# Performance work log

Measured on AMD Instinct MI355X. Metric: run time of the kernel, lower is better.

The kernel has to match this reference:

```python
import jax, jax.numpy as jnp
import numpy as np

N_NODES = 100000
N_EDGES = 1600000
D = 64
N_TARGETS = 100
N_GRAPHS = 512


def gcn_conv(x, W, b, src, dst):
    """GCNConv with default add_self_loops=True, symmetric normalization."""
    n = x.shape[0]
    h = x @ W  # [N, out]
    ones = jnp.ones(dst.shape[0], dtype=h.dtype)
    deg = jax.ops.segment_sum(ones, dst, num_segments=n) + 1.0  # +1 for self-loop
    dinv = jax.lax.rsqrt(deg)
    norm = dinv[src] * dinv[dst]  # [E]
    agg = jax.ops.segment_sum(h[src] * norm[:, None], dst, num_segments=n)
    agg = agg + h * (dinv * dinv)[:, None]  # self-loop contribution: 1/deg[i] * h[i]
    return agg + b


def setup_inputs() -> dict:
    key = jax.random.key(0)
    ks = jax.random.split(key, 12)
    x = jax.random.normal(ks[0], (N_NODES, D), dtype=jnp.float32)
    edge_index = jax.random.randint(ks[1], (2, N_EDGES), 0, N_NODES, dtype=jnp.int64)
    batch_seg = jnp.sort(jax.random.randint(ks[2], (N_NODES,), 0, N_GRAPHS, dtype=jnp.int64))
    s = 1.0 / np.sqrt(D)
    W1 = jax.random.normal(ks[3], (D, D), dtype=jnp.float32) * s
    b1 = jnp.zeros((D,), dtype=jnp.float32)
    W2 = jax.random.normal(ks[4], (D, D), dtype=jnp.float32) * s
    b2 = jnp.zeros((D,), dtype=jnp.float32)
    W3 = jax.random.normal(ks[5], (D, D), dtype=jnp.float32) * s
    b3 = jnp.zeros((D,), dtype=jnp.float32)
    Wout = jax.random.normal(ks[6], (D, N_TARGETS), dtype=jnp.float32) * s
    bout = jnp.zeros((N_TARGETS,), dtype=jnp.float32)
    return {"x": x, "W1": W1, "b1": b1, "W2": W2, "b2": b2, "W3": W3, "b3": b3,
            "Wout": Wout, "bout": bout, "edge_index": edge_index, "batch_seg": batch_seg}


def reference(x, W1, b1, W2, b2, W3, b3, Wout, bout, edge_index, batch_seg):
    src, dst = edge_index[0], edge_index[1]
    h = jax.nn.relu(gcn_conv(x, W1, b1, src, dst))   # dropout p=0 -> identity
    h = jax.nn.relu(gcn_conv(h, W2, b2, src, dst))
    h = gcn_conv(h, W3, b3, src, dst)
    counts = jax.ops.segment_sum(jnp.ones(h.shape[0], h.dtype), batch_seg, num_segments=N_GRAPHS)
    pooled = jax.ops.segment_sum(h, batch_seg, num_segments=N_GRAPHS) / jnp.maximum(counts, 1.0)[:, None]
    return pooled @ Wout + bout  # [N_GRAPHS, N_TARGETS]
```

## Files before the change

kernel.cpp:

```cpp
#include <hip/hip_runtime.h>

#define N_NODES   100000
#define N_EDGES   1600000
#define D         64
#define N_TARGETS 100
#define N_GRAPHS  512
#define NBUCK     391
#define EPB       4096
#define BCAP      6144
#define MM_NPW    16
#define NPN       4

typedef _Float16 half4 __attribute__((ext_vector_type(4)));
typedef _Float16 half8 __attribute__((ext_vector_type(8)));
typedef __fp16   hf2   __attribute__((ext_vector_type(2)));
typedef __fp16   hf8   __attribute__((ext_vector_type(8)));

#if defined(__has_builtin)
#if __has_builtin(__builtin_amdgcn_fdot2)
#define USE_DOT2 1
#endif
#endif

__global__ void k_init(int* __restrict__ gcur, float* __restrict__ poolz) {
    int i = blockIdx.x * blockDim.x + threadIdx.x;
    if (i < NBUCK) gcur[i] = 0;
    if (i < N_GRAPHS * D + N_GRAPHS) poolz[i] = 0.0f;
}

__global__ void k_prepW(const float* __restrict__ W, _Float16* __restrict__ out) {
    int t = threadIdx.x;
#pragma unroll
    for (int it = 0; it < 2; ++it) {
        int idx = t + it * 256;
        int m = idx >> 3, c = idx & 7;
        half8 hv;
#pragma unroll
        for (int tt = 0; tt < 8; ++tt)
            hv[tt] = (_Float16)W[(8 * c + tt) * 64 + m];
        *(half8*)&out[m * 64 + ((c ^ (m & 7)) * 8)] = hv;
    }
}

__global__ void __launch_bounds__(256)
k_binA(const int* __restrict__ src, const int* __restrict__ dst,
       int* __restrict__ gcur, unsigned long long* __restrict__ staged) {
    __shared__ int hist[NBUCK];
    __shared__ int boff[NBUCK];
    int tid = threadIdx.x;
    for (int i = tid; i < NBUCK; i += 256) hist[i] = 0;
    __syncthreads();

    int e0 = blockIdx.x * EPB;
    int s_[16], d_[16], r_[16];
#pragma unroll
    for (int k = 0; k < 16; ++k) {
        int e = e0 + k * 256 + tid;
        if (e < N_EDGES) {
            s_[k] = src[e];
            d_[k] = dst[e];
            r_[k] = atomicAdd(&hist[d_[k] >> 8], 1);
        } else {
            d_[k] = -1;
        }
    }
    __syncthreads();
    for (int b = tid; b < NBUCK; b += 256) {
        int h = hist[b];
        boff[b] = (h > 0) ? atomicAdd(&gcur[b], h) : 0;
    }
    __syncthreads();
#pragma unroll
    for (int k = 0; k < 16; ++k) {
        if (d_[k] >= 0) {
            int b = d_[k] >> 8;
            staged[(size_t)b * BCAP + boff[b] + r_[k]] =
                ((unsigned long long)(unsigned)d_[k] << 32) | (unsigned)s_[k];
        }
    }
}

__global__ void k_scanB(const int* __restrict__ gcur, int* __restrict__ bstart) {
    __shared__ int s[512];
    int t = threadIdx.x;
    int v = (t < NBUCK) ? gcur[t] : 0;
    s[t] = v;
    __syncthreads();
    for (int off = 1; off < 512; off <<= 1) {
        int x = (t >= off) ? s[t - off] : 0;
        __syncthreads();
        s[t] += x;
        __syncthreads();
    }
    if (t < NBUCK) bstart[t] = s[t] - v;
    if (t == 0) bstart[NBUCK] = N_EDGES;
}

__global__ void __launch_bounds__(256)
k_binB(const unsigned long long* __restrict__ staged, const int* __restrict__ gcur,
       const int* __restrict__ bstart, int* __restrict__ esrc,
       int* __restrict__ base, float* __restrict__ dinv) {
    __shared__ int s[256];
    __shared__ int lbase[256];
    __shared__ int cur[256];
    int b = blockIdx.x;
    int t = threadIdx.x;
    int n0 = b << 8;
    int Eb = gcur[b];
    int Sb = bstart[b];
    const unsigned long long* sl = staged + (size_t)b * BCAP;

    cur[t] = 0;
    __syncthreads();
    for (int k = t; k < Eb; k += 256) {
        int dl = ((int)(sl[k] >> 32)) & 255;
        atomicAdd(&cur[dl], 1);
    }
    __syncthreads();
    int v = cur[t];
    s[t] = v;
    __syncthreads();
    for (int off = 1; off < 256; off <<= 1) {
        int x = (t >= off) ? s[t - off] : 0;
        __syncthreads();
        s[t] += x;
        __syncthreads();
    }
    lbase[t] = s[t] - v;
    int gi = n0 + t;
    if (gi < N_NODES) {
        base[gi] = Sb + (s[t] - v);
        dinv[gi] = rsqrtf((float)v + 1.0f);
    }
    if (b == 0 && t == 0) base[N_NODES] = N_EDGES;
    cur[t] = 0;
    __syncthreads();
    for (int k = t; k < Eb; k += 256) {
        unsigned long long pd = sl[k];
        int dl = ((int)(pd >> 32)) & 255;
        int pos = Sb + lbase[dl] + atomicAdd(&cur[dl], 1);
        esrc[pos] = (int)(pd & 0xffffffffu);
    }
}

__global__ void __launch_bounds__(256)
k_mm(const float* __restrict__ X, const float* __restrict__ W,
     const float* __restrict__ dinv, _Float16* __restrict__ Y16) {
    __shared__ float W1L[D * D];
    __shared__ float aSh[4][D];
    int tid = threadIdx.x;
#pragma unroll
    for (int it = 0; it < 4; ++it) {
        int idx = (tid + it * 256) * 4;
        *(float4*)&W1L[idx] = *(const float4*)(W + idx);
    }
    __syncthreads();

    int wv = tid >> 6, lane = tid & 63;
    float wreg[D];
#pragma unroll
    for (int k = 0; k < D; ++k)
        wreg[k] = W1L[k * D + lane];

    int i0 = (blockIdx.x * 4 + wv) * MM_NPW;
    if (i0 >= N_NODES) return;
    int iEnd = i0 + MM_NPW; if (iEnd > N_NODES) iEnd = N_NODES;

    float xv = X[(size_t)i0 * D + lane];
    for (int i = i0; i < iEnd; ++i) {
        int inext = (i + 1 < N_NODES) ? (i + 1) : i;
        float xnext = X[(size_t)inext * D + lane];

        aSh[wv][lane] = xv;
        asm volatile("s_waitcnt lgkmcnt(0)" ::: "memory");

        float ac0 = 0.f, ac1 = 0.f, ac2 = 0.f, ac3 = 0.f;
#pragma unroll
        for (int c = 0; c < 16; ++c) {
            float4 a4 = *(const float4*)&aSh[wv][c * 4];
            ac0 = fmaf(a4.x, wreg[4 * c + 0], ac0);
            ac1 = fmaf(a4.y, wreg[4 * c + 1], ac1);
            ac2 = fmaf(a4.z, wreg[4 * c + 2], ac2);
            ac3 = fmaf(a4.w, wreg[4 * c + 3], ac3);
        }
        float acc = (ac0 + ac1) + (ac2 + ac3);
        Y16[(size_t)i * D + lane] = (_Float16)(acc * dinv[i]);
        xv = xnext;
    }
}

__global__ void __launch_bounds__(256)
k_pullmm(const _Float16* __restrict__ H, const int* __restrict__ esrc,
         const int* __restrict__ base, const float* __restrict__ dinv,
         const float* __restrict__ b_in, const _Float16* __restrict__ Whg,
         _Float16* __restrict__ Hout) {
    __shared__ _Float16 WhL[D * D];
    __shared__ float    red[4][8][D + 4];
    __shared__ _Float16 aSh[4][D];
    {
#pragma unroll
        for (int it = 0; it < 2; ++it) {
            int t = threadIdx.x + it * 256;
            *(half8*)&WhL[t * 8] = *(const half8*)&Whg[t * 8];
        }
    }
    __syncthreads();

    int wv   = threadIdx.x >> 6;
    int lane = threadIdx.x & 63;
    int g = lane >> 3, l = lane & 7;
    float bias = b_in[lane];
    int i0 = (blockIdx.x * 4 + wv) * NPN;

    for (int n = 0; n < NPN; ++n) {
        int i = i0 + n;
        int s0 = base[i], s1 = base[i + 1];

        float acc[8] = {0.f, 0.f, 0.f, 0.f, 0.f, 0.f, 0.f, 0.f};
        if (g == 0) {
            half8 sv = *(const half8*)(H + (size_t)i * D + l * 8);
#pragma unroll
            for (int q = 0; q < 8; ++q) acc[q] = (float)sv[q];
        }

        int p = s0;
        while (p < s1) {
            int cnt = s1 - p;
            if (cnt > 64) cnt = 64;
            int ed = (lane < cnt) ? esrc[p + lane] : 0;
            int j = 0;
            for (; j + 32 <= cnt; j += 32) {
                int e0 = __shfl(ed, j + g, 64);
                int e1 = __shfl(ed, j + 8 + g, 64);
                int e2 = __shfl(ed, j + 16 + g, 64);
                int e3 = __shfl(ed, j + 24 + g, 64);
                half8 v0 = *(const half8*)(H + (size_t)(unsigned)e0 * D + l * 8);
                half8 v1 = *(const half8*)(H + (size_t)(unsigned)e1 * D + l * 8);
                half8 v2 = *(const half8*)(H + (size_t)(unsigned)e2 * D + l * 8);
                half8 v3 = *(const half8*)(H + (size_t)(unsigned)e3 * D + l * 8);
                half8 s01 = v0 + v1;
                half8 s23 = v2 + v3;
#pragma unroll
                for (int q = 0; q < 8; ++q)
                    acc[q] += (float)s01[q] + (float)s23[q];
            }
            for (; j + 16 <= cnt; j += 16) {
                int e0 = __shfl(ed, j + g, 64);
                int e1 = __shfl(ed, j + 8 + g, 64);
                half8 v0 = *(const half8*)(H + (size_t)(unsigned)e0 * D + l * 8);
                half8 v1 = *(const half8*)(H + (size_t)(unsigned)e1 * D + l * 8);
                half8 s01 = v0 + v1;
#pragma unroll
                for (int q = 0; q < 8; ++q) acc[q] += (float)s01[q];
            }
            for (; j + 8 <= cnt; j += 8) {
                int e0 = __shfl(ed, j + g, 64);
                half8 v0 = *(const half8*)(H + (size_t)(unsigned)e0 * D + l * 8);
#pragma unroll
                for (int q = 0; q < 8; ++q) acc[q] += (float)v0[q];
            }
            if (j < cnt) {
                int idx = j + g;
                int e0 = __shfl(ed, idx & 63, 64);
                if (idx < cnt) {
                    half8 v0 = *(const half8*)(H + (size_t)(unsigned)e0 * D + l * 8);
#pragma unroll
                    for (int q = 0; q < 8; ++q) acc[q] += (float)v0[q];
                }
            }
            p += cnt;
        }

        *(float4*)&red[wv][g][l * 8]     = make_float4(acc[0], acc[1], acc[2], acc[3]);
        *(float4*)&red[wv][g][l * 8 + 4] = make_float4(acc[4], acc[5], acc[6], acc[7]);
        asm volatile("s_waitcnt lgkmcnt(0)" ::: "memory");
        float agg = 0.f;
#pragma unroll
        for (int gg = 0; gg < 8; ++gg)
            agg += red[wv][gg][lane];

        float di = dinv[i];
        float av = fmaxf(fmaf(agg, di, bias), 0.f);
        aSh[wv][lane] = (_Float16)av;
        asm volatile("s_waitcnt lgkmcnt(0)" ::: "memory");

        float part = 0.f;
#pragma unroll
        for (int c = 0; c < 8; ++c) {
            hf8 a8 = *(const hf8*)&aSh[wv][c * 8];
            hf8 w8 = *(const hf8*)&WhL[lane * 64 + ((c ^ (lane & 7)) * 8)];
#ifdef USE_DOT2
#pragma unroll
            for (int q = 0; q < 4; ++q) {
                hf2 ap; ap.x = a8[2 * q]; ap.y = a8[2 * q + 1];
                hf2 wp; wp.x = w8[2 * q]; wp.y = w8[2 * q + 1];
                part = __builtin_amdgcn_fdot2(ap, wp, part, false);
            }
#else
#pragma unroll
            for (int t = 0; t < 8; ++t)
                part = fmaf((float)a8[t], (float)w8[t], part);
#endif
        }
        Hout[(size_t)i * D + lane] = (_Float16)(part * di);
    }
}

__global__ void __launch_bounds__(256)
k_pull(const _Float16* __restrict__ H, const int* __restrict__ esrc,
       const int* __restrict__ base, const float* __restrict__ dinv,
       const float* __restrict__ b, _Float16* __restrict__ AGG16) {
    __shared__ float red[4][8][D + 4];
    int wv   = threadIdx.x >> 6;
    int lane = threadIdx.x & 63;
    int g = lane >> 3, l = lane & 7;
    float bias = b[lane];
    int i0 = (blockIdx.x * 4 + wv) * NPN;

    for (int n = 0; n < NPN; ++n) {
        int i = i0 + n;
        int s0 = base[i], s1 = base[i + 1];

        float acc[8] = {0.f, 0.f, 0.f, 0.f, 0.f, 0.f, 0.f, 0.f};
        if (g == 0) {
            half8 sv = *(const half8*)(H + (size_t)i * D + l * 8);
#pragma unroll
            for (int q = 0; q < 8; ++q) acc[q] = (float)sv[q];
        }

        int p = s0;
        while (p < s1) {
            int cnt = s1 - p;
            if (cnt > 64) cnt = 64;
            int ed = (lane < cnt) ? esrc[p + lane] : 0;
            int j = 0;
            for (; j + 32 <= cnt; j += 32) {
                int e0 = __shfl(ed, j + g, 64);
                int e1 = __shfl(ed, j + 8 + g, 64);
                int e2 = __shfl(ed, j + 16 + g, 64);
                int e3 = __shfl(ed, j + 24 + g, 64);
                half8 v0 = *(const half8*)(H + (size_t)(unsigned)e0 * D + l * 8);
                half8 v1 = *(const half8*)(H + (size_t)(unsigned)e1 * D + l * 8);
                half8 v2 = *(const half8*)(H + (size_t)(unsigned)e2 * D + l * 8);
                half8 v3 = *(const half8*)(H + (size_t)(unsigned)e3 * D + l * 8);
                half8 s01 = v0 + v1;
                half8 s23 = v2 + v3;
#pragma unroll
                for (int q = 0; q < 8; ++q)
                    acc[q] += (float)s01[q] + (float)s23[q];
            }
            for (; j + 16 <= cnt; j += 16) {
                int e0 = __shfl(ed, j + g, 64);
                int e1 = __shfl(ed, j + 8 + g, 64);
                half8 v0 = *(const half8*)(H + (size_t)(unsigned)e0 * D + l * 8);
                half8 v1 = *(const half8*)(H + (size_t)(unsigned)e1 * D + l * 8);
                half8 s01 = v0 + v1;
#pragma unroll
                for (int q = 0; q < 8; ++q) acc[q] += (float)s01[q];
            }
            for (; j + 8 <= cnt; j += 8) {
                int e0 = __shfl(ed, j + g, 64);
                half8 v0 = *(const half8*)(H + (size_t)(unsigned)e0 * D + l * 8);
#pragma unroll
                for (int q = 0; q < 8; ++q) acc[q] += (float)v0[q];
            }
            if (j < cnt) {
                int idx = j + g;
                int e0 = __shfl(ed, idx & 63, 64);
                if (idx < cnt) {
                    half8 v0 = *(const half8*)(H + (size_t)(unsigned)e0 * D + l * 8);
#pragma unroll
                    for (int q = 0; q < 8; ++q) acc[q] += (float)v0[q];
                }
            }
            p += cnt;
        }

        *(float4*)&red[wv][g][l * 8]     = make_float4(acc[0], acc[1], acc[2], acc[3]);
        *(float4*)&red[wv][g][l * 8 + 4] = make_float4(acc[4], acc[5], acc[6], acc[7]);
        asm volatile("s_waitcnt lgkmcnt(0)" ::: "memory");
        float agg = 0.f;
#pragma unroll
        for (int gg = 0; gg < 8; ++gg)
            agg += red[wv][gg][lane];
        asm volatile("s_waitcnt lgkmcnt(0)" ::: "memory");

        AGG16[(size_t)i * D + lane] = (_Float16)fmaf(agg, dinv[i], bias);
    }
}

__global__ void __launch_bounds__(256)
k_pool_seg(const _Float16* __restrict__ H16, const int* __restrict__ seg,
           float* __restrict__ pooled, float* __restrict__ counts) {
    int wave = threadIdx.x >> 6;
    int lane = threadIdx.x & 63;
    int n0 = (blockIdx.x * 4 + wave) * 64;
    if (n0 >= N_NODES) return;
    int nEnd = n0 + 64;
    if (nEnd > N_NODES) nEnd = N_NODES;
    int cur = seg[n0];
    float acc = 0.0f;
    int run = 0;
    for (int n = n0; n < nEnd; ++n) {
        int gsg = seg[n];
        if (gsg != cur) {
            atomicAdd(&pooled[(size_t)cur * D + lane], acc);
            if (lane == 0) atomicAdd(&counts[cur], (float)run);
            acc = 0.0f; run = 0;
            cur = gsg;
        }
        acc += (float)H16[(size_t)n * D + lane];
        run += 1;
    }
    atomicAdd(&pooled[(size_t)cur * D + lane], acc);
    if (lane == 0) atomicAdd(&counts[cur], (float)run);
}

__global__ void k_out(const float* __restrict__ pooled, const float* __restrict__ counts,
                      const float* __restrict__ Wout, const float* __restrict__ bout,
                      float* __restrict__ out) {
    __shared__ float prow[D];
    int g = blockIdx.x;
    int t = threadIdx.x;
    if (t < D) prow[t] = pooled[(size_t)g * D + t] / fmaxf(counts[g], 1.0f);
    __syncthreads();
    if (t < N_TARGETS) {
        float acc = bout[t];
#pragma unroll
        for (int k = 0; k < D; ++k)
            acc = fmaf(prow[k], Wout[k * N_TARGETS + t], acc);
        out[g * N_TARGETS + t] = acc;
    }
}


extern "C" void kernel_launch(void* const* d_in, const int* in_sizes, int n_in,
                              void* d_out, int out_size, void* d_ws, size_t ws_size,
                              hipStream_t stream) {
    const float* x    = (const float*)d_in[0];
    const float* W1   = (const float*)d_in[1];
    const float* b1   = (const float*)d_in[2];
    const float* W2   = (const float*)d_in[3];
    const float* b2   = (const float*)d_in[4];
    const float* W3   = (const float*)d_in[5];
    const float* b3   = (const float*)d_in[6];
    const float* Wout = (const float*)d_in[7];
    const float* bout = (const float*)d_in[8];
    const int*   eidx = (const int*)d_in[9];
    const int*   seg  = (const int*)d_in[10];
    const int* src = eidx;
    const int* dst = eidx + N_EDGES;
    float* out = (float*)d_out;

    _Float16* H16A   = (_Float16*)d_ws;
    _Float16* H16B   = H16A + (size_t)N_NODES * D;
    _Float16* AGG16  = H16B;
    unsigned long long* staged = (unsigned long long*)d_ws;
    int*      esrc   = (int*)(H16B + (size_t)N_NODES * D);
    float*    dinv   = (float*)(esrc + N_EDGES);
    int*      base   = (int*)(dinv + N_NODES);
    float*    pooled = (float*)(base + N_NODES + 4);
    float*    counts = pooled + N_GRAPHS * D;
    int*      gcur   = (int*)(counts + N_GRAPHS);
    int*      bstart = gcur + 512;
    _Float16* WhA    = (_Float16*)(bstart + 512);
    _Float16* WhB    = WhA + 4096;

    const int NB = (N_NODES + 255) / 256;

    k_prepW<<<1, 256, 0, stream>>>(W2, WhA);
    k_prepW<<<1, 256, 0, stream>>>(W3, WhB);

    k_init<<<130, 256, 0, stream>>>(gcur, pooled);
    k_binA<<<(N_EDGES + EPB - 1) / EPB, 256, 0, stream>>>(src, dst, gcur, staged);
    k_scanB<<<1, 512, 0, stream>>>(gcur, bstart);
    k_binB<<<NBUCK, 256, 0, stream>>>(staged, gcur, bstart, esrc, base, dinv);

    const int MMB = (N_NODES + 4 * MM_NPW - 1) / (4 * MM_NPW);
    const int PB  = N_NODES / (4 * NPN);
    k_mm<<<MMB, 256, 0, stream>>>(x, W1, dinv, H16A);
    k_pullmm<<<PB, 256, 0, stream>>>(H16A, esrc, base, dinv, b1, WhA, H16B);
    k_pullmm<<<PB, 256, 0, stream>>>(H16B, esrc, base, dinv, b2, WhB, H16A);
    k_pull<<<PB, 256, 0, stream>>>(H16A, esrc, base, dinv, b3, AGG16);

    k_pool_seg<<<NB, 256, 0, stream>>>(AGG16, seg, pooled, counts);
    k_out<<<N_GRAPHS, 128, 0, stream>>>(pooled, counts, Wout, bout, out);
}
```

Measured before the change: 320.2 us.

## Fuse mean-pool into final pull kernel and prefetch next node's edges

The last aggregation kernel now accumulates each node's output directly into per-graph pooled sums with atomics, so the fp16 intermediate buffer and the separate pooling kernel go away. Both pull kernels also preload all node base offsets and prefetch the next node's edge-index chunk and self row while the current node is processed, to hide gather latency. In exchange, the number of pooling atomics grows, since each wave flushes after only four nodes, which adds contention on the pooled rows.

```diff
diff --git a/kernel.cpp b/kernel.cpp
--- a/kernel.cpp
+++ b/kernel.cpp
@@ -212,22 +212,37 @@
     float bias = b_in[lane];
     int i0 = (blockIdx.x * 4 + wv) * NPN;
 
+    int bv[NPN + 1];
+#pragma unroll
+    for (int q = 0; q <= NPN; ++q) bv[q] = base[i0 + q];
+
+    int pc0 = bv[1] - bv[0]; if (pc0 > 64) pc0 = 64;
+    int edn = (lane < pc0) ? esrc[bv[0] + lane] : 0;
+    half8 svn = *(const half8*)(H + (size_t)i0 * D + l * 8);
+
+#pragma unroll
     for (int n = 0; n < NPN; ++n) {
         int i = i0 + n;
-        int s0 = base[i], s1 = base[i + 1];
+        int s0 = bv[n], s1 = bv[n + 1];
+        int ed0 = edn;
+        half8 sv = svn;
+
+        if (n + 1 < NPN) {
+            int pcN = bv[n + 2] - bv[n + 1]; if (pcN > 64) pcN = 64;
+            edn = (lane < pcN) ? esrc[bv[n + 1] + lane] : 0;
+            svn = *(const half8*)(H + (size_t)(i + 1) * D + l * 8);
+        }
 
         float acc[8] = {0.f, 0.f, 0.f, 0.f, 0.f, 0.f, 0.f, 0.f};
         if (g == 0) {
-            half8 sv = *(const half8*)(H + (size_t)i * D + l * 8);
 #pragma unroll
             for (int q = 0; q < 8; ++q) acc[q] = (float)sv[q];
         }
 
         int p = s0;
+        int cnt = s1 - p; if (cnt > 64) cnt = 64;
+        int ed = ed0;
         while (p < s1) {
-            int cnt = s1 - p;
-            if (cnt > 64) cnt = 64;
-            int ed = (lane < cnt) ? esrc[p + lane] : 0;
             int j = 0;
             for (; j + 32 <= cnt; j += 32) {
                 int e0 = __shfl(ed, j + g, 64);
@@ -269,6 +284,9 @@
                 }
             }
             p += cnt;
+            if (p >= s1) break;
+            cnt = s1 - p; if (cnt > 64) cnt = 64;
+            ed = (lane < cnt) ? esrc[p + lane] : 0;
         }
 
         *(float4*)&red[wv][g][l * 8]     = make_float4(acc[0], acc[1], acc[2], acc[3]);
@@ -309,7 +327,8 @@
 __global__ void __launch_bounds__(256)
 k_pull(const _Float16* __restrict__ H, const int* __restrict__ esrc,
        const int* __restrict__ base, const float* __restrict__ dinv,
-       const float* __restrict__ b, _Float16* __restrict__ AGG16) {
+       const float* __restrict__ b, const int* __restrict__ seg,
+       float* __restrict__ pooled, float* __restrict__ counts) {
     __shared__ float red[4][8][D + 4];
     int wv   = threadIdx.x >> 6;
     int lane = threadIdx.x & 63;
@@ -317,22 +336,44 @@
     float bias = b[lane];
     int i0 = (blockIdx.x * 4 + wv) * NPN;
 
+    int bv[NPN + 1];
+#pragma unroll
+    for (int q = 0; q <= NPN; ++q) bv[q] = base[i0 + q];
+    int sgv[NPN];
+#pragma unroll
+    for (int q = 0; q < NPN; ++q) sgv[q] = seg[i0 + q];
+
+    int pc0 = bv[1] - bv[0]; if (pc0 > 64) pc0 = 64;
+    int edn = (lane < pc0) ? esrc[bv[0] + lane] : 0;
+    half8 svn = *(const half8*)(H + (size_t)i0 * D + l * 8);
+
+    int   curs = sgv[0];
+    float poolacc = 0.f;
+    int   run = 0;
+
+#pragma unroll
     for (int n = 0; n < NPN; ++n) {
         int i = i0 + n;
-        int s0 = base[i], s1 = base[i + 1];
+        int s0 = bv[n], s1 = bv[n + 1];
+        int ed0 = edn;
+        half8 sv = svn;
+
+        if (n + 1 < NPN) {
+            int pcN = bv[n + 2] - bv[n + 1]; if (pcN > 64) pcN = 64;
+            edn = (lane < pcN) ? esrc[bv[n + 1] + lane] : 0;
+            svn = *(const half8*)(H + (size_t)(i + 1) * D + l * 8);
+        }
 
         float acc[8] = {0.f, 0.f, 0.f, 0.f, 0.f, 0.f, 0.f, 0.f};
         if (g == 0) {
-            half8 sv = *(const half8*)(H + (size_t)i * D + l * 8);
 #pragma unroll
             for (int q = 0; q < 8; ++q) acc[q] = (float)sv[q];
         }
 
         int p = s0;
+        int cnt = s1 - p; if (cnt > 64) cnt = 64;
+        int ed = ed0;
         while (p < s1) {
-            int cnt = s1 - p;
-            if (cnt > 64) cnt = 64;
-            int ed = (lane < cnt) ? esrc[p + lane] : 0;
             int j = 0;
             for (; j + 32 <= cnt; j += 32) {
                 int e0 = __shfl(ed, j + g, 64);
@@ -374,6 +415,9 @@
                 }
             }
             p += cnt;
+            if (p >= s1) break;
+            cnt = s1 - p; if (cnt > 64) cnt = 64;
+            ed = (lane < cnt) ? esrc[p + lane] : 0;
         }
 
         *(float4*)&red[wv][g][l * 8]     = make_float4(acc[0], acc[1], acc[2], acc[3]);
@@ -385,35 +429,17 @@
             agg += red[wv][gg][lane];
         asm volatile("s_waitcnt lgkmcnt(0)" ::: "memory");
 
-        AGG16[(size_t)i * D + lane] = (_Float16)fmaf(agg, dinv[i], bias);
-    }
-}
-
-__global__ void __launch_bounds__(256)
-k_pool_seg(const _Float16* __restrict__ H16, const int* __restrict__ seg,
-           float* __restrict__ pooled, float* __restrict__ counts) {
-    int wave = threadIdx.x >> 6;
-    int lane = threadIdx.x & 63;
-    int n0 = (blockIdx.x * 4 + wave) * 64;
-    if (n0 >= N_NODES) return;
-    int nEnd = n0 + 64;
-    if (nEnd > N_NODES) nEnd = N_NODES;
-    int cur = seg[n0];
-    float acc = 0.0f;
-    int run = 0;
-    for (int n = n0; n < nEnd; ++n) {
-        int gsg = seg[n];
-        if (gsg != cur) {
-            atomicAdd(&pooled[(size_t)cur * D + lane], acc);
-            if (lane == 0) atomicAdd(&counts[cur], (float)run);
-            acc = 0.0f; run = 0;
-            cur = gsg;
-        }
-        acc += (float)H16[(size_t)n * D + lane];
-        run += 1;
-    }
-    atomicAdd(&pooled[(size_t)cur * D + lane], acc);
-    if (lane == 0) atomicAdd(&counts[cur], (float)run);
+        float val = fmaf(agg, dinv[i], bias);
+
+        if (sgv[n] != curs) {
+            atomicAdd(&pooled[(size_t)curs * D + lane], poolacc);
+            if (lane == 0) atomicAdd(&counts[curs], (float)run);
+            poolacc = 0.f; run = 0; curs = sgv[n];
+        }
+        poolacc += val; run += 1;
+    }
+    atomicAdd(&pooled[(size_t)curs * D + lane], poolacc);
+    if (lane == 0) atomicAdd(&counts[curs], (float)run);
 }
 
 __global__ void k_out(const float* __restrict__ pooled, const float* __restrict__ counts,
@@ -454,7 +480,6 @@
 
     _Float16* H16A   = (_Float16*)d_ws;
     _Float16* H16B   = H16A + (size_t)N_NODES * D;
-    _Float16* AGG16  = H16B;
     unsigned long long* staged = (unsigned long long*)d_ws;
     int*      esrc   = (int*)(H16B + (size_t)N_NODES * D);
     float*    dinv   = (float*)(esrc + N_EDGES);
@@ -466,8 +491,6 @@
     _Float16* WhA    = (_Float16*)(bstart + 512);
     _Float16* WhB    = WhA + 4096;
 
-    const int NB = (N_NODES + 255) / 256;
-
     k_prepW<<<1, 256, 0, stream>>>(W2, WhA);
     k_prepW<<<1, 256, 0, stream>>>(W3, WhB);
 
@@ -481,8 +504,7 @@
     k_mm<<<MMB, 256, 0, stream>>>(x, W1, dinv, H16A);
     k_pullmm<<<PB, 256, 0, stream>>>(H16A, esrc, base, dinv, b1, WhA, H16B);
     k_pullmm<<<PB, 256, 0, stream>>>(H16B, esrc, base, dinv, b2, WhB, H16A);
-    k_pull<<<PB, 256, 0, stream>>>(H16A, esrc, base, dinv, b3, AGG16);
-
-    k_pool_seg<<<NB, 256, 0, stream>>>(AGG16, seg, pooled, counts);
+    k_pull<<<PB, 256, 0, stream>>>(H16A, esrc, base, dinv, b3, seg, pooled, counts);
+
     k_out<<<N_GRAPHS, 128, 0, stream>>>(pooled, counts, Wout, bout, out);
 }
```

Result: slower. 360.2 us (+12.5%).
